# Performance work log

Hardware: AMD Instinct MI355X
Metric: run time of the kernel (lower is better)

## Reference

```python
import jax, jax.numpy as jnp
import numpy as np

# Constants matching init_kwargs
N_HEADS = 8
D_MODEL = 256
PATCH_NUM = 128
D_K = D_MODEL // N_HEADS  # 32
TEMP = 0.5
EPS = 1e-10


def setup_inputs() -> dict:
    key = jax.random.key(0)
    ks = jax.random.split(key, 20)
    s = 0.02
    d, h, n = D_MODEL, N_HEADS, PATCH_NUM
    inp = {
        "x": jax.random.normal(ks[0], (32, n, d), dtype=jnp.float32),
        "gumbel_u": jax.random.uniform(ks[1], (h, n, n, 2), dtype=jnp.float32),
        "memory_w": jax.random.normal(ks[2], (n, h * d), dtype=jnp.float32) * s,
        "fc_out_w": jax.random.normal(ks[3], (2 * d, d), dtype=jnp.float32) * s,
        "fc_out_b": jnp.zeros((d,), jnp.float32),
        "fc_cat_w": jax.random.normal(ks[4], (d, 2), dtype=jnp.float32) * s,
        "fc_cat_b": jnp.zeros((2,), jnp.float32),
        "wq": jax.random.normal(ks[5], (d, d), dtype=jnp.float32) * s,
        "bq": jnp.zeros((d,), jnp.float32),
        "wk": jax.random.normal(ks[6], (d, d), dtype=jnp.float32) * s,
        "bk": jnp.zeros((d,), jnp.float32),
        "wv": jax.random.normal(ks[7], (d, d), dtype=jnp.float32) * s,
        "bv": jnp.zeros((d,), jnp.float32),
        "out_w": jax.random.normal(ks[8], (d, d), dtype=jnp.float32) * s,
        "out_b": jnp.zeros((d,), jnp.float32),
        "mlp_w1": jax.random.normal(ks[9], (d, d), dtype=jnp.float32) * s,
        "mlp_b1": jnp.zeros((d,), jnp.float32),
        "mlp_w2": jax.random.normal(ks[10], (d, d), dtype=jnp.float32) * s,
        "mlp_b2": jnp.zeros((d,), jnp.float32),
    }
    return inp


def _forward(x, memory_w, fc_out_w, fc_out_b, fc_cat_w, fc_cat_b,
             wq, bq, wk, bk, wv, bv, out_w, out_b,
             mlp_w1, mlp_b1, mlp_w2, mlp_b2, gumbel_u):
    H, N, D = N_HEADS, PATCH_NUM, D_MODEL
    B = x.shape[0]

    # ---- SSConnectionLearning on memory feats ----
    # memory: Embedding(N, d_model*n_heads) -> feats [H, N, D]
    feats = memory_w.reshape(N, H, D).transpose(1, 0, 2)
    # rel_rec gathers row index i (receiver), rel_send gathers col index j (sender)
    senders = jnp.broadcast_to(feats[:, None, :, :], (H, N, N, D))   # feats[j]
    receivers = jnp.broadcast_to(feats[:, :, None, :], (H, N, N, D))  # feats[i]
    pair = jnp.concatenate([senders, receivers], axis=-1)  # [H,N,N,2D]
    hdn = jax.nn.relu(jnp.einsum('hijc,cd->hijd', pair, fc_out_w) + fc_out_b)
    logits = jnp.einsum('hijd,dk->hijk', hdn, fc_cat_w) + fc_cat_b  # [H,N,N,2]

    # gumbel-softmax, hard=True, straight-through
    g = -jnp.log(-jnp.log(gumbel_u + EPS) + EPS)
    y_soft = jax.nn.softmax((logits + g) / TEMP, axis=-1)
    y_hard = jax.nn.one_hot(jnp.argmax(y_soft, axis=-1), 2, dtype=y_soft.dtype)
    y = jax.lax.stop_gradient(y_hard - y_soft) + y_soft
    conn = y[..., 1]  # [H,N,N] learned sparse connection mask

    # ---- PatchIntegration (GELU MLP, dropout = identity in eval) ----
    xm = jax.nn.gelu(x @ mlp_w1 + mlp_b1)
    xm = xm @ mlp_w2 + mlp_b2

    # ---- Multihead attention masked by connection matrix ----
    q = (xm @ wq + bq).reshape(B, N, H, D_K).transpose(0, 2, 1, 3)  # [B,H,N,dk]
    k = (xm @ wk + bk).reshape(B, N, H, D_K).transpose(0, 2, 1, 3)
    v = (xm @ wv + bv).reshape(B, N, H, D_K).transpose(0, 2, 1, 3)
    scale = D_K ** -0.5
    scores = jnp.einsum('bhqd,bhkd->bhqk', q, k) * scale
    # additive mask: blocked where conn==0 (large negative keeps softmax finite)
    scores = scores + (conn[None] - 1.0) * 1e9
    attn = jax.nn.softmax(scores, axis=-1)
    out = jnp.einsum('bhqk,bhkd->bhqd', attn, v)
    out = out.transpose(0, 2, 1, 3).reshape(B, N, H * D_K)
    out = out @ out_w + out_b
    return out


def reference(x, gumbel_u, memory_w, fc_out_w, fc_out_b, fc_cat_w, fc_cat_b,
              wq, bq, wk, bk, wv, bv, out_w, out_b,
              mlp_w1, mlp_b1, mlp_w2, mlp_b2):
    return _forward(x, memory_w, fc_out_w, fc_out_b, fc_cat_w, fc_cat_b,
                    wq, bq, wk, bk, wv, bv, out_w, out_b,
                    mlp_w1, mlp_b1, mlp_w2, mlp_b2, gumbel_u)
```

## Files before the change

### kernel.cpp

```cpp
#include <hip/hip_runtime.h>
#include <hip/hip_bf16.h>
#include <math.h>


typedef short short8 __attribute__((ext_vector_type(8)));
typedef float f32x4 __attribute__((ext_vector_type(4)));

union V8 { uint4 u; short8 s; };

__device__ __forceinline__ float gelu_f(float x) {
    float inner = 0.7978845608028654f * (x + 0.044715f * x * x * x);
    return 0.5f * x * (1.0f + tanhf(inner));
}
__device__ __forceinline__ void split_bf16(float x, ushort& h, ushort& l) {
    __hip_bfloat16 bh = __float2bfloat16(x);
    float hf = __bfloat162float(bh);
    __hip_bfloat16 bl = __float2bfloat16(x - hf);
    h = __builtin_bit_cast(ushort, bh);
    l = __builtin_bit_cast(ushort, bl);
}
__device__ __forceinline__ ushort bf16bits(float x) {
    return __builtin_bit_cast(ushort, __float2bfloat16(x));
}
__device__ __forceinline__ float bits_to_f(ushort v) {
    return __builtin_bit_cast(float, ((uint)v) << 16);
}
__device__ __forceinline__ short8 lds_frag(const ushort* p) {
    V8 v; v.u = *(const uint4*)p; return v.s;
}


__global__ __launch_bounds__(512) void k_wprep(
    const float* __restrict__ mlp_w1, const float* __restrict__ mlp_w2,
    const float* __restrict__ wq, const float* __restrict__ wk,
    const float* __restrict__ wv, const float* __restrict__ out_w,
    const float* __restrict__ fc_out_w,
    ushort* __restrict__ hi, ushort* __restrict__ lo) {
    __shared__ __align__(16) float xs2[2][32 * 132];
    int bx = blockIdx.x, t = threadIdx.x;
    int half = t >> 8, tl = t & 255;
    int job = bx * 2 + half;
    int m = job >> 4, ks = (job >> 1) & 7, nh = job & 1;
    const float* W = m == 0 ? mlp_w1 : m == 1 ? mlp_w2 : m == 2 ? wq :
                     m == 3 ? wk : m == 4 ? wv : m == 5 ? out_w :
                     m == 6 ? fc_out_w : fc_out_w + 65536;
    ushort* Hm = hi + m * 65536;
    ushort* Lm = lo + m * 65536;
    float* xs = xs2[half];
    #pragma unroll
    for (int p = 0; p < 4; ++p) {
        int idx = p * 256 + tl;
        int row = idx >> 5, c4 = (idx & 31) * 4;
        *(float4*)(xs + row * 132 + c4) =
            *(const float4*)(W + (ks * 32 + row) * 256 + nh * 128 + c4);
    }
    __syncthreads();
    int lane = tl & 63, lr = lane & 15, quad = lane >> 4;
    #pragma unroll
    for (int it = 0; it < 2; ++it) {
        int tgl = (tl >> 6) + 4 * it;
        int tg = nh * 8 + tgl;
        int nl = tgl * 16 + lr;
        ushort hb[8], lb[8];
        #pragma unroll
        for (int j = 0; j < 8; ++j)
            split_bf16(xs[(quad * 8 + j) * 132 + nl], hb[j], lb[j]);
        uint4 ph = { (uint)hb[0] | ((uint)hb[1] << 16), (uint)hb[2] | ((uint)hb[3] << 16),
                     (uint)hb[4] | ((uint)hb[5] << 16), (uint)hb[6] | ((uint)hb[7] << 16) };
        uint4 pl = { (uint)lb[0] | ((uint)lb[1] << 16), (uint)lb[2] | ((uint)lb[3] << 16),
                     (uint)lb[4] | ((uint)lb[5] << 16), (uint)lb[6] | ((uint)lb[7] << 16) };
        int idx = ((tg * 8 + ks) * 64 + lane) * 8;
        *(uint4*)(Hm + idx) = ph;
        *(uint4*)(Lm + idx) = pl;
    }
}

__global__ __launch_bounds__(512) void k_p2(
    const float* __restrict__ memory_w, const float* __restrict__ X,
    const ushort* __restrict__ Whi, const ushort* __restrict__ Wlo,
    const float* __restrict__ b1, const float* __restrict__ b2,
    const float* __restrict__ Bq, const float* __restrict__ Bk,
    const float* __restrict__ Bv,
    float* __restrict__ A, float* __restrict__ Bm,
    ushort* __restrict__ Q, ushort* __restrict__ K, ushort* __restrict__ V) {
    __shared__ __align__(16) union {
        struct { ushort xhi[16 * 264], xlo[16 * 264]; } f;
        struct {
            ushort aHi[16 * 264], aLo[16 * 264];
            ushort bHi[16 * 264], bLo[16 * 264];
        } g;
    } sm;
    int bx = blockIdx.x, t = threadIdx.x;
    if (bx < 64) {
        int rt = bx;
        #pragma unroll
        for (int ii = 0; ii < 2; ++ii) {
            int f4 = ii * 512 + t;
            int rr = f4 >> 6, c = (f4 & 63) * 4;
            int r = rt * 16 + rr;
            int h = r >> 7, n = r & 127;
            float4 xv = *(const float4*)(memory_w + n * 2048 + h * 256 + c);
            ushort hh[4], ll[4];
            split_bf16(xv.x, hh[0], ll[0]); split_bf16(xv.y, hh[1], ll[1]);
            split_bf16(xv.z, hh[2], ll[2]); split_bf16(xv.w, hh[3], ll[3]);
            uint2 ph = { (uint)hh[0] | ((uint)hh[1] << 16), (uint)hh[2] | ((uint)hh[3] << 16) };
            uint2 pl = { (uint)ll[0] | ((uint)ll[1] << 16), (uint)ll[2] | ((uint)ll[3] << 16) };
            *(uint2*)(sm.f.xhi + rr * 264 + c) = ph;
            *(uint2*)(sm.f.xlo + rr * 264 + c) = pl;
        }
        __syncthreads();
        int lane = t & 63, w = t >> 6;
        int lr = lane & 15, quad = lane >> 4;
        int msel = w & 1, cq = w >> 1;
        const uint4* H4 = (const uint4*)(Whi + (6 + msel) * 65536);
        const uint4* L4 = (const uint4*)(Wlo + (6 + msel) * 65536);
        const ushort* ah = sm.f.xhi + lr * 264 + quad * 8;
        const ushort* al = sm.f.xlo + lr * 264 + quad * 8;
        float* O = msel ? Bm : A;
        #pragma unroll
        for (int i = 0; i < 4; ++i) {
            int tg = cq * 4 + i;
            f32x4 acc = {};
            #pragma unroll
            for (int ks = 0; ks < 8; ++ks) {
                short8 a_h = lds_frag(ah + ks * 32);
                short8 a_l = lds_frag(al + ks * 32);
                int off = (tg * 8 + ks) * 64 + lane;
                V8 bh, bl; bh.u = H4[off]; bl.u = L4[off];
                acc = __builtin_amdgcn_mfma_f32_16x16x32_bf16(a_h, bh.s, acc, 0, 0, 0);
                acc = __builtin_amdgcn_mfma_f32_16x16x32_bf16(a_l, bh.s, acc, 0, 0, 0);
                acc = __builtin_amdgcn_mfma_f32_16x16x32_bf16(a_h, bl.s, acc, 0, 0, 0);
            }
            int n0 = tg * 16 + lr;
            #pragma unroll
            for (int r = 0; r < 4; ++r)
                O[(rt * 16 + quad * 4 + r) * 256 + n0] = acc[r];
        }
        return;
    }
    int r0 = (bx - 64) * 16;
    #pragma unroll
    for (int ii = 0; ii < 2; ++ii) {
        int f4 = ii * 512 + t;
        int row = f4 >> 6, c = (f4 & 63) * 4;
        float4 xv = *(const float4*)(X + (r0 + row) * 256 + c);
        ushort h[4], l[4];
        split_bf16(xv.x, h[0], l[0]); split_bf16(xv.y, h[1], l[1]);
        split_bf16(xv.z, h[2], l[2]); split_bf16(xv.w, h[3], l[3]);
        uint2 ph = { (uint)h[0] | ((uint)h[1] << 16), (uint)h[2] | ((uint)h[3] << 16) };
        uint2 pl = { (uint)l[0] | ((uint)l[1] << 16), (uint)l[2] | ((uint)l[3] << 16) };
        *(uint2*)(sm.g.aHi + row * 264 + c) = ph;
        *(uint2*)(sm.g.aLo + row * 264 + c) = pl;
    }
    __syncthreads();
    int lane = t & 63, w = t >> 6;
    int lr = lane & 15, quad = lane >> 4;
    int aoff = lr * 264 + quad * 8;
    {
        const uint4* H4 = (const uint4*)(Whi + 0 * 65536);
        const uint4* L4 = (const uint4*)(Wlo + 0 * 65536);
        f32x4 acc[2] = {};
        #pragma unroll
        for (int ks = 0; ks < 8; ++ks) {
            short8 a_h = lds_frag(sm.g.aHi + aoff + ks * 32);
            short8 a_l = lds_frag(sm.g.aLo + aoff + ks * 32);
            #pragma unroll
            for (int ti = 0; ti < 2; ++ti) {
                int off = ((w * 2 + ti) * 8 + ks) * 64 + lane;
                V8 bh, bl; bh.u = H4[off]; bl.u = L4[off];
                acc[ti] = __builtin_amdgcn_mfma_f32_16x16x32_bf16(a_h, bh.s, acc[ti], 0, 0, 0);
                acc[ti] = __builtin_amdgcn_mfma_f32_16x16x32_bf16(a_l, bh.s, acc[ti], 0, 0, 0);
                acc[ti] = __builtin_amdgcn_mfma_f32_16x16x32_bf16(a_h, bl.s, acc[ti], 0, 0, 0);
            }
        }
        #pragma unroll
        for (int ti = 0; ti < 2; ++ti) {
            int n0 = (w * 2 + ti) * 16 + lr;
            float bb = b1[n0];
            #pragma unroll
            for (int r = 0; r < 4; ++r) {
                float o = gelu_f(acc[ti][r] + bb);
                ushort hh, ll; split_bf16(o, hh, ll);
                int ad = (quad * 4 + r) * 264 + n0;
                sm.g.bHi[ad] = hh; sm.g.bLo[ad] = ll;
            }
        }
    }
    __syncthreads();
    {
        const uint4* H4 = (const uint4*)(Whi + 1 * 65536);
        const uint4* L4 = (const uint4*)(Wlo + 1 * 65536);
        f32x4 acc[2] = {};
        #pragma unroll
        for (int ks = 0; ks < 8; ++ks) {
            short8 a_h = lds_frag(sm.g.bHi + aoff + ks * 32);
            short8 a_l = lds_frag(sm.g.bLo + aoff + ks * 32);
            #pragma unroll
            for (int ti = 0; ti < 2; ++ti) {
                int off = ((w * 2 + ti) * 8 + ks) * 64 + lane;
                V8 bh, bl; bh.u = H4[off]; bl.u = L4[off];
                acc[ti] = __builtin_amdgcn_mfma_f32_16x16x32_bf16(a_h, bh.s, acc[ti], 0, 0, 0);
                acc[ti] = __builtin_amdgcn_mfma_f32_16x16x32_bf16(a_l, bh.s, acc[ti], 0, 0, 0);
                acc[ti] = __builtin_amdgcn_mfma_f32_16x16x32_bf16(a_h, bl.s, acc[ti], 0, 0, 0);
            }
        }
        __syncthreads();
        #pragma unroll
        for (int ti = 0; ti < 2; ++ti) {
            int n0 = (w * 2 + ti) * 16 + lr;
            float bb = b2[n0];
            #pragma unroll
            for (int r = 0; r < 4; ++r) {
                float o = acc[ti][r] + bb;
                ushort hh, ll; split_bf16(o, hh, ll);
                int ad = (quad * 4 + r) * 264 + n0;
                sm.g.aHi[ad] = hh; sm.g.aLo[ad] = ll;
            }
        }
    }
    __syncthreads();
    {
        const uint4* Hq = (const uint4*)(Whi + 2 * 65536);
        const uint4* Lq = (const uint4*)(Wlo + 2 * 65536);
        const uint4* Hk = (const uint4*)(Whi + 3 * 65536);
        const uint4* Lk = (const uint4*)(Wlo + 3 * 65536);
        const uint4* Hv = (const uint4*)(Whi + 4 * 65536);
        const uint4* Lv = (const uint4*)(Wlo + 4 * 65536);
        f32x4 aq[2] = {}, ak[2] = {}, av[2] = {};
        #pragma unroll 2
        for (int ks = 0; ks < 8; ++ks) {
            short8 a_h = lds_frag(sm.g.aHi + aoff + ks * 32);
            short8 a_l = lds_frag(sm.g.aLo + aoff + ks * 32);
            #pragma unroll
            for (int ti = 0; ti < 2; ++ti) {
                int off = ((w * 2 + ti) * 8 + ks) * 64 + lane;
                V8 qh, ql, kh, kl, vh, vl;
                qh.u = Hq[off]; ql.u = Lq[off];
                kh.u = Hk[off]; kl.u = Lk[off];
                vh.u = Hv[off]; vl.u = Lv[off];
                aq[ti] = __builtin_amdgcn_mfma_f32_16x16x32_bf16(a_h, qh.s, aq[ti], 0, 0, 0);
                aq[ti] = __builtin_amdgcn_mfma_f32_16x16x32_bf16(a_l, qh.s, aq[ti], 0, 0, 0);
                aq[ti] = __builtin_amdgcn_mfma_f32_16x16x32_bf16(a_h, ql.s, aq[ti], 0, 0, 0);
                ak[ti] = __builtin_amdgcn_mfma_f32_16x16x32_bf16(a_h, kh.s, ak[ti], 0, 0, 0);
                ak[ti] = __builtin_amdgcn_mfma_f32_16x16x32_bf16(a_l, kh.s, ak[ti], 0, 0, 0);
                ak[ti] = __builtin_amdgcn_mfma_f32_16x16x32_bf16(a_h, kl.s, ak[ti], 0, 0, 0);
                av[ti] = __builtin_amdgcn_mfma_f32_16x16x32_bf16(a_h, vh.s, av[ti], 0, 0, 0);
                av[ti] = __builtin_amdgcn_mfma_f32_16x16x32_bf16(a_l, vh.s, av[ti], 0, 0, 0);
                av[ti] = __builtin_amdgcn_mfma_f32_16x16x32_bf16(a_h, vl.s, av[ti], 0, 0, 0);
            }
        }
        #pragma unroll
        for (int ti = 0; ti < 2; ++ti) {
            int n0 = (w * 2 + ti) * 16 + lr;
            float bq = Bq[n0], bk = Bk[n0], bv = Bv[n0];
            #pragma unroll
            for (int r = 0; r < 4; ++r) {
                int go = (r0 + quad * 4 + r) * 256 + n0;
                Q[go] = bf16bits(aq[ti][r] + bq);
                K[go] = bf16bits(ak[ti][r] + bk);
                V[go] = bf16bits(av[ti][r] + bv);
            }
        }
    }
}

__global__ __launch_bounds__(512) void k_conn(
    const float* __restrict__ A, const float* __restrict__ Bmat,
    const float* __restrict__ fc_out_b, const float* __restrict__ fc_cat_w,
    const float* __restrict__ fc_cat_b, const float* __restrict__ gumbel_u,
    ushort* __restrict__ maskb) {
    __shared__ __align__(16) float sA[16 * 260], sB[32 * 260];
    int bx = blockIdx.x, t = threadIdx.x;
    int h = bx >> 5;
    int rem = bx & 31;
    int it = rem >> 3, jt = rem & 7;
    int i0 = it * 32, j0 = jt * 16;
    int jl = t & 15, il = t >> 4;
    #pragma unroll
    for (int p = 0; p < 6; ++p) {
        int id2 = p * 512 + t;
        if (id2 < 1024) {
            int rr = id2 >> 6, c = (id2 & 63) * 4;
            *(float4*)(sA + rr * 260 + c) =
                *(const float4*)(A + (h * 128 + j0 + rr) * 256 + c);
        } else {
            int id3 = id2 - 1024;
            int rr = id3 >> 6, c = (id3 & 63) * 4;
            float4 bv = *(const float4*)(Bmat + (h * 128 + i0 + rr) * 256 + c);
            float4 fb = *(const float4*)(fc_out_b + c);
            bv.x += fb.x; bv.y += fb.y; bv.z += fb.z; bv.w += fb.w;
            *(float4*)(sB + rr * 260 + c) = bv;
        }
    }
    __syncthreads();
    const float* Ar = sA + jl * 260;
    const float* Br = sB + il * 260;
    float l0 = fc_cat_b[0], l1 = fc_cat_b[1];
    #pragma unroll 4
    for (int d4 = 0; d4 < 64; ++d4) {
        int d = d4 * 4;
        float4 av = *(const float4*)(Ar + d);
        float4 bv = *(const float4*)(Br + d);
        float4 cwA = *(const float4*)(fc_cat_w + d * 2);
        float4 cwB = *(const float4*)(fc_cat_w + d * 2 + 4);
        float h0 = fmaxf(av.x + bv.x, 0.f);
        float h1 = fmaxf(av.y + bv.y, 0.f);
        float h2 = fmaxf(av.z + bv.z, 0.f);
        float h3 = fmaxf(av.w + bv.w, 0.f);
        l0 += h0 * cwA.x + h1 * cwA.z + h2 * cwB.x + h3 * cwB.z;
        l1 += h0 * cwA.y + h1 * cwA.w + h2 * cwB.y + h3 * cwB.w;
    }
    int i = i0 + il, j = j0 + jl;
    float2 uu = *(const float2*)(gumbel_u + ((h * 128 + i) * 128 + j) * 2);
    float g0 = -logf(-logf(uu.x + 1e-10f) + 1e-10f);
    float g1 = -logf(-logf(uu.y + 1e-10f) + 1e-10f);
    bool on = (l1 + g1) > (l0 + g0);
    maskb[(h * 128 + i) * 128 + j] = bf16bits(on ? 0.f : -1e9f);
}

__global__ __launch_bounds__(256) void k_attn_mfma(
    const ushort* __restrict__ Q, const ushort* __restrict__ K,
    const ushort* __restrict__ V, const ushort* __restrict__ maskb,
    float* __restrict__ AO) {
    int bx = blockIdx.x;
    int b = bx >> 4, h = (bx >> 1) & 7, rh = bx & 1;
    int t = threadIdx.x;
    int lane = t & 63, w = t >> 6;
    __shared__ __align__(16) ushort vT[32 * 136];
    __shared__ __align__(16) ushort ps[64 * 136];
    #pragma unroll
    for (int it = 0; it < 2; ++it) {
        int idx = it * 256 + t;
        int key = idx >> 2, dq8 = (idx & 3) * 8;
        V8 vv; vv.u = *(const uint4*)(V + (b * 128 + key) * 256 + h * 32 + dq8);
        #pragma unroll
        for (int m = 0; m < 8; ++m)
            vT[(dq8 + m) * 136 + key] = (ushort)vv.s[m];
    }
    __syncthreads();
    int lr = lane & 15, quad = lane >> 4;
    int rt = rh * 4 + w;
    V8 af;
    af.u = *(const uint4*)(Q + (b * 128 + rt * 16 + lr) * 256 + h * 32 + quad * 8);
    f32x4 s[8];
    #pragma unroll
    for (int ct = 0; ct < 8; ++ct) {
        V8 bf_;
        bf_.u = *(const uint4*)(K + (b * 128 + ct * 16 + lr) * 256 + h * 32 + quad * 8);
        f32x4 z = {0.f, 0.f, 0.f, 0.f};
        s[ct] = __builtin_amdgcn_mfma_f32_16x16x32_bf16(af.s, bf_.s, z, 0, 0, 0);
    }
    const float scale = 0.17677669529663687f;
    const ushort* mrow = maskb + h * 16384;
    #pragma unroll
    for (int r = 0; r < 4; ++r) {
        int lrow = w * 16 + quad * 4 + r;
        int grow = rt * 16 + quad * 4 + r;
        float sv[8];
        float mx = -3.0e38f;
        #pragma unroll
        for (int ct = 0; ct < 8; ++ct) {
            float bias = bits_to_f(mrow[grow * 128 + ct * 16 + lr]);
            sv[ct] = s[ct][r] * scale + bias;
            mx = fmaxf(mx, sv[ct]);
        }
        mx = fmaxf(mx, __shfl_xor(mx, 1));
        mx = fmaxf(mx, __shfl_xor(mx, 2));
        mx = fmaxf(mx, __shfl_xor(mx, 4));
        mx = fmaxf(mx, __shfl_xor(mx, 8));
        float sum = 0.f;
        #pragma unroll
        for (int ct = 0; ct < 8; ++ct) {
            sv[ct] = __expf(sv[ct] - mx);
            sum += sv[ct];
        }
        sum += __shfl_xor(sum, 1);
        sum += __shfl_xor(sum, 2);
        sum += __shfl_xor(sum, 4);
        sum += __shfl_xor(sum, 8);
        float iv = 1.f / sum;
        #pragma unroll
        for (int ct = 0; ct < 8; ++ct)
            ps[lrow * 136 + ct * 16 + lr] = bf16bits(sv[ct] * iv);
    }
    f32x4 o0 = {}, o1 = {};
    #pragma unroll
    for (int kk = 0; kk < 4; ++kk) {
        short8 pa = lds_frag(ps + (w * 16 + lr) * 136 + kk * 32 + quad * 8);
        short8 v0 = lds_frag(vT + lr * 136 + kk * 32 + quad * 8);
        short8 v1 = lds_frag(vT + (16 + lr) * 136 + kk * 32 + quad * 8);
        o0 = __builtin_amdgcn_mfma_f32_16x16x32_bf16(pa, v0, o0, 0, 0, 0);
        o1 = __builtin_amdgcn_mfma_f32_16x16x32_bf16(pa, v1, o1, 0, 0, 0);
    }
    #pragma unroll
    for (int r = 0; r < 4; ++r) {
        int grow = rt * 16 + quad * 4 + r;
        float* op = AO + b * 32768 + grow * 256 + h * 32;
        op[lr] = o0[r];
        op[16 + lr] = o1[r];
    }
}

__global__ __launch_bounds__(256) void k_gemm16(
    const float* __restrict__ X, const ushort* __restrict__ Whi,
    const ushort* __restrict__ Wlo, const float* __restrict__ bias,
    float* __restrict__ Y) {
    __shared__ __align__(16) ushort xhi[16 * 264], xlo[16 * 264];
    int t = threadIdx.x;
    int r0 = blockIdx.x * 16;
    #pragma unroll
    for (int ii = 0; ii < 4; ++ii) {
        int f4 = ii * 256 + t;
        int row = f4 >> 6, c = (f4 & 63) * 4;
        float4 xv = *(const float4*)(X + (r0 + row) * 256 + c);
        ushort h[4], l[4];
        split_bf16(xv.x, h[0], l[0]); split_bf16(xv.y, h[1], l[1]);
        split_bf16(xv.z, h[2], l[2]); split_bf16(xv.w, h[3], l[3]);
        uint2 ph = { (uint)h[0] | ((uint)h[1] << 16), (uint)h[2] | ((uint)h[3] << 16) };
        uint2 pl = { (uint)l[0] | ((uint)l[1] << 16), (uint)l[2] | ((uint)l[3] << 16) };
        *(uint2*)(xhi + row * 264 + c) = ph;
        *(uint2*)(xlo + row * 264 + c) = pl;
    }
    __syncthreads();
    int l = t & 63, w = t >> 6;
    int lr = l & 15, quad = l >> 4;
    int tg = blockIdx.y * 4 + w;
    const ushort* ah = xhi + lr * 264 + quad * 8;
    const ushort* al = xlo + lr * 264 + quad * 8;
    const uint4* H4 = (const uint4*)Whi;
    const uint4* L4 = (const uint4*)Wlo;
    f32x4 acc = {};
    #pragma unroll
    for (int ks = 0; ks < 8; ++ks) {
        short8 a_h = lds_frag(ah + ks * 32);
        short8 a_l = lds_frag(al + ks * 32);
        int off = (tg * 8 + ks) * 64 + l;
        V8 bh, bl; bh.u = H4[off]; bl.u = L4[off];
        acc = __builtin_amdgcn_mfma_f32_16x16x32_bf16(a_h, bh.s, acc, 0, 0, 0);
        acc = __builtin_amdgcn_mfma_f32_16x16x32_bf16(a_l, bh.s, acc, 0, 0, 0);
        acc = __builtin_amdgcn_mfma_f32_16x16x32_bf16(a_h, bl.s, acc, 0, 0, 0);
    }
    int n0 = tg * 16 + lr;
    float bs = bias[n0];
    #pragma unroll
    for (int r = 0; r < 4; ++r)
        Y[(r0 + quad * 4 + r) * 256 + n0] = acc[r] + bs;
}

extern "C" void kernel_launch(void* const* d_in, const int* in_sizes, int n_in,
                              void* d_out, int out_size, void* d_ws, size_t ws_size,
                              hipStream_t stream) {
    const float* x        = (const float*)d_in[0];
    const float* gumbel_u = (const float*)d_in[1];
    const float* memory_w = (const float*)d_in[2];
    const float* fc_out_w = (const float*)d_in[3];
    const float* fc_out_b = (const float*)d_in[4];
    const float* fc_cat_w = (const float*)d_in[5];
    const float* fc_cat_b = (const float*)d_in[6];
    const float* wq       = (const float*)d_in[7];
    const float* bq       = (const float*)d_in[8];
    const float* wk       = (const float*)d_in[9];
    const float* bk       = (const float*)d_in[10];
    const float* wv_      = (const float*)d_in[11];
    const float* bv_      = (const float*)d_in[12];
    const float* out_w    = (const float*)d_in[13];
    const float* out_b    = (const float*)d_in[14];
    const float* mlp_w1   = (const float*)d_in[15];
    const float* mlp_b1   = (const float*)d_in[16];
    const float* mlp_w2   = (const float*)d_in[17];
    const float* mlp_b2   = (const float*)d_in[18];

    float* ws    = (float*)d_ws;
    float* A     = ws;
    float* Bm    = ws + 262144;
    ushort* mask = (ushort*)(ws + 524288);
    ushort* qb   = (ushort*)(ws + 589824);
    ushort* kb   = (ushort*)(ws + 1114112);
    ushort* vb   = (ushort*)(ws + 1638400);
    float* ao    = ws + 2162688;
    ushort* wf_hi = (ushort*)(ws + 3211264);
    ushort* wf_lo = wf_hi + 8 * 65536;
    float* out   = (float*)d_out;

    k_wprep<<<dim3(64), dim3(512), 0, stream>>>(
        mlp_w1, mlp_w2, wq, wk, wv_, out_w, fc_out_w, wf_hi, wf_lo);
    k_p2<<<dim3(320), dim3(512), 0, stream>>>(
        memory_w, x, wf_hi, wf_lo, mlp_b1, mlp_b2, bq, bk, bv_,
        A, Bm, qb, kb, vb);
    k_conn<<<dim3(256), dim3(512), 0, stream>>>(
        A, Bm, fc_out_b, fc_cat_w, fc_cat_b, gumbel_u, mask);
    k_attn_mfma<<<dim3(512), dim3(256), 0, stream>>>(qb, kb, vb, mask, ao);
    k_gemm16<<<dim3(256, 4), dim3(256), 0, stream>>>(ao, wf_hi + 5 * 65536,
                                                     wf_lo + 5 * 65536, out_b, out);
}
```

Before: 144.7 us.

## Regroup kernels: merge weight prep with memory GEMM, fuse MLP/QKV with conn mask

The launch sequence is restructured from five kernels into four. The first kernel now splits the six square weights into bf16 hi/lo and also computes the memory-feature GEMMs (A, Bm), reading and splitting fc_out_w directly from fp32 in-loop instead of using pre-split weights. The second kernel runs the MLP/QKV projection and the connection-mask computation as independent block ranges, which removes one launch and one dependency barrier. The cost is strided, uncoalesced fp32 loads of fc_out_w with redundant splitting in the memory GEMM blocks, and a larger union in shared memory for the fused kernel.

```diff
diff --git a/kernel.cpp b/kernel.cpp
--- a/kernel.cpp
+++ b/kernel.cpp
@@ -30,69 +30,55 @@
 }
 
 
-__global__ __launch_bounds__(512) void k_wprep(
+__global__ __launch_bounds__(512) void k_d1(
     const float* __restrict__ mlp_w1, const float* __restrict__ mlp_w2,
     const float* __restrict__ wq, const float* __restrict__ wk,
     const float* __restrict__ wv, const float* __restrict__ out_w,
-    const float* __restrict__ fc_out_w,
-    ushort* __restrict__ hi, ushort* __restrict__ lo) {
-    __shared__ __align__(16) float xs2[2][32 * 132];
-    int bx = blockIdx.x, t = threadIdx.x;
-    int half = t >> 8, tl = t & 255;
-    int job = bx * 2 + half;
-    int m = job >> 4, ks = (job >> 1) & 7, nh = job & 1;
-    const float* W = m == 0 ? mlp_w1 : m == 1 ? mlp_w2 : m == 2 ? wq :
-                     m == 3 ? wk : m == 4 ? wv : m == 5 ? out_w :
-                     m == 6 ? fc_out_w : fc_out_w + 65536;
-    ushort* Hm = hi + m * 65536;
-    ushort* Lm = lo + m * 65536;
-    float* xs = xs2[half];
-    #pragma unroll
-    for (int p = 0; p < 4; ++p) {
-        int idx = p * 256 + tl;
-        int row = idx >> 5, c4 = (idx & 31) * 4;
-        *(float4*)(xs + row * 132 + c4) =
-            *(const float4*)(W + (ks * 32 + row) * 256 + nh * 128 + c4);
-    }
-    __syncthreads();
-    int lane = tl & 63, lr = lane & 15, quad = lane >> 4;
-    #pragma unroll
-    for (int it = 0; it < 2; ++it) {
-        int tgl = (tl >> 6) + 4 * it;
-        int tg = nh * 8 + tgl;
-        int nl = tgl * 16 + lr;
-        ushort hb[8], lb[8];
-        #pragma unroll
-        for (int j = 0; j < 8; ++j)
-            split_bf16(xs[(quad * 8 + j) * 132 + nl], hb[j], lb[j]);
-        uint4 ph = { (uint)hb[0] | ((uint)hb[1] << 16), (uint)hb[2] | ((uint)hb[3] << 16),
-                     (uint)hb[4] | ((uint)hb[5] << 16), (uint)hb[6] | ((uint)hb[7] << 16) };
-        uint4 pl = { (uint)lb[0] | ((uint)lb[1] << 16), (uint)lb[2] | ((uint)lb[3] << 16),
-                     (uint)lb[4] | ((uint)lb[5] << 16), (uint)lb[6] | ((uint)lb[7] << 16) };
-        int idx = ((tg * 8 + ks) * 64 + lane) * 8;
-        *(uint4*)(Hm + idx) = ph;
-        *(uint4*)(Lm + idx) = pl;
-    }
-}
-
-__global__ __launch_bounds__(512) void k_p2(
-    const float* __restrict__ memory_w, const float* __restrict__ X,
-    const ushort* __restrict__ Whi, const ushort* __restrict__ Wlo,
-    const float* __restrict__ b1, const float* __restrict__ b2,
-    const float* __restrict__ Bq, const float* __restrict__ Bk,
-    const float* __restrict__ Bv,
-    float* __restrict__ A, float* __restrict__ Bm,
-    ushort* __restrict__ Q, ushort* __restrict__ K, ushort* __restrict__ V) {
+    const float* __restrict__ fc_out_w, const float* __restrict__ memory_w,
+    ushort* __restrict__ hi, ushort* __restrict__ lo,
+    float* __restrict__ A, float* __restrict__ Bm) {
     __shared__ __align__(16) union {
+        float xs[2][32 * 132];
         struct { ushort xhi[16 * 264], xlo[16 * 264]; } f;
-        struct {
-            ushort aHi[16 * 264], aLo[16 * 264];
-            ushort bHi[16 * 264], bLo[16 * 264];
-        } g;
     } sm;
     int bx = blockIdx.x, t = threadIdx.x;
-    if (bx < 64) {
-        int rt = bx;
+    if (bx < 48) {
+        int half = t >> 8, tl = t & 255;
+        int job = bx * 2 + half;
+        int m = job >> 4, ks = (job >> 1) & 7, nh = job & 1;
+        const float* W = m == 0 ? mlp_w1 : m == 1 ? mlp_w2 : m == 2 ? wq :
+                         m == 3 ? wk : m == 4 ? wv : out_w;
+        ushort* Hm = hi + m * 65536;
+        ushort* Lm = lo + m * 65536;
+        float* xs = sm.xs[half];
+        #pragma unroll
+        for (int p = 0; p < 4; ++p) {
+            int idx = p * 256 + tl;
+            int row = idx >> 5, c4 = (idx & 31) * 4;
+            *(float4*)(xs + row * 132 + c4) =
+                *(const float4*)(W + (ks * 32 + row) * 256 + nh * 128 + c4);
+        }
+        __syncthreads();
+        int lane = tl & 63, lr = lane & 15, quad = lane >> 4;
+        #pragma unroll
+        for (int it = 0; it < 2; ++it) {
+            int tgl = (tl >> 6) + 4 * it;
+            int tg = nh * 8 + tgl;
+            int nl = tgl * 16 + lr;
+            ushort hb[8], lb[8];
+            #pragma unroll
+            for (int j = 0; j < 8; ++j)
+                split_bf16(xs[(quad * 8 + j) * 132 + nl], hb[j], lb[j]);
+            uint4 ph = { (uint)hb[0] | ((uint)hb[1] << 16), (uint)hb[2] | ((uint)hb[3] << 16),
+                         (uint)hb[4] | ((uint)hb[5] << 16), (uint)hb[6] | ((uint)hb[7] << 16) };
+            uint4 pl = { (uint)lb[0] | ((uint)lb[1] << 16), (uint)lb[2] | ((uint)lb[3] << 16),
+                         (uint)lb[4] | ((uint)lb[5] << 16), (uint)lb[6] | ((uint)lb[7] << 16) };
+            int idx = ((tg * 8 + ks) * 64 + lane) * 8;
+            *(uint4*)(Hm + idx) = ph;
+            *(uint4*)(Lm + idx) = pl;
+        }
+    } else {
+        int rt = bx - 48;
         #pragma unroll
         for (int ii = 0; ii < 2; ++ii) {
             int f4 = ii * 512 + t;
@@ -112,210 +98,231 @@
         int lane = t & 63, w = t >> 6;
         int lr = lane & 15, quad = lane >> 4;
         int msel = w & 1, cq = w >> 1;
-        const uint4* H4 = (const uint4*)(Whi + (6 + msel) * 65536);
-        const uint4* L4 = (const uint4*)(Wlo + (6 + msel) * 65536);
+        const float* Wf = fc_out_w + msel * 65536;
         const ushort* ah = sm.f.xhi + lr * 264 + quad * 8;
         const ushort* al = sm.f.xlo + lr * 264 + quad * 8;
         float* O = msel ? Bm : A;
         #pragma unroll
         for (int i = 0; i < 4; ++i) {
             int tg = cq * 4 + i;
+            int n = tg * 16 + lr;
             f32x4 acc = {};
             #pragma unroll
             for (int ks = 0; ks < 8; ++ks) {
                 short8 a_h = lds_frag(ah + ks * 32);
                 short8 a_l = lds_frag(al + ks * 32);
-                int off = (tg * 8 + ks) * 64 + lane;
-                V8 bh, bl; bh.u = H4[off]; bl.u = L4[off];
+                int k0 = ks * 32 + quad * 8;
+                V8 bh, bl;
+                #pragma unroll
+                for (int j = 0; j < 8; ++j) {
+                    ushort hh, ll;
+                    split_bf16(Wf[(k0 + j) * 256 + n], hh, ll);
+                    bh.s[j] = (short)hh;
+                    bl.s[j] = (short)ll;
+                }
                 acc = __builtin_amdgcn_mfma_f32_16x16x32_bf16(a_h, bh.s, acc, 0, 0, 0);
                 acc = __builtin_amdgcn_mfma_f32_16x16x32_bf16(a_l, bh.s, acc, 0, 0, 0);
                 acc = __builtin_amdgcn_mfma_f32_16x16x32_bf16(a_h, bl.s, acc, 0, 0, 0);
             }
-            int n0 = tg * 16 + lr;
             #pragma unroll
             for (int r = 0; r < 4; ++r)
-                O[(rt * 16 + quad * 4 + r) * 256 + n0] = acc[r];
-        }
-        return;
-    }
-    int r0 = (bx - 64) * 16;
-    #pragma unroll
-    for (int ii = 0; ii < 2; ++ii) {
-        int f4 = ii * 512 + t;
-        int row = f4 >> 6, c = (f4 & 63) * 4;
-        float4 xv = *(const float4*)(X + (r0 + row) * 256 + c);
-        ushort h[4], l[4];
-        split_bf16(xv.x, h[0], l[0]); split_bf16(xv.y, h[1], l[1]);
-        split_bf16(xv.z, h[2], l[2]); split_bf16(xv.w, h[3], l[3]);
-        uint2 ph = { (uint)h[0] | ((uint)h[1] << 16), (uint)h[2] | ((uint)h[3] << 16) };
-        uint2 pl = { (uint)l[0] | ((uint)l[1] << 16), (uint)l[2] | ((uint)l[3] << 16) };
-        *(uint2*)(sm.g.aHi + row * 264 + c) = ph;
-        *(uint2*)(sm.g.aLo + row * 264 + c) = pl;
-    }
-    __syncthreads();
-    int lane = t & 63, w = t >> 6;
-    int lr = lane & 15, quad = lane >> 4;
-    int aoff = lr * 264 + quad * 8;
-    {
-        const uint4* H4 = (const uint4*)(Whi + 0 * 65536);
-        const uint4* L4 = (const uint4*)(Wlo + 0 * 65536);
-        f32x4 acc[2] = {};
-        #pragma unroll
-        for (int ks = 0; ks < 8; ++ks) {
-            short8 a_h = lds_frag(sm.g.aHi + aoff + ks * 32);
-            short8 a_l = lds_frag(sm.g.aLo + aoff + ks * 32);
-            #pragma unroll
-            for (int ti = 0; ti < 2; ++ti) {
-                int off = ((w * 2 + ti) * 8 + ks) * 64 + lane;
-                V8 bh, bl; bh.u = H4[off]; bl.u = L4[off];
-                acc[ti] = __builtin_amdgcn_mfma_f32_16x16x32_bf16(a_h, bh.s, acc[ti], 0, 0, 0);
-                acc[ti] = __builtin_amdgcn_mfma_f32_16x16x32_bf16(a_l, bh.s, acc[ti], 0, 0, 0);
-                acc[ti] = __builtin_amdgcn_mfma_f32_16x16x32_bf16(a_h, bl.s, acc[ti], 0, 0, 0);
-            }
-        }
-        #pragma unroll
-        for (int ti = 0; ti < 2; ++ti) {
-            int n0 = (w * 2 + ti) * 16 + lr;
-            float bb = b1[n0];
-            #pragma unroll
-            for (int r = 0; r < 4; ++r) {
-                float o = gelu_f(acc[ti][r] + bb);
-                ushort hh, ll; split_bf16(o, hh, ll);
-                int ad = (quad * 4 + r) * 264 + n0;
-                sm.g.bHi[ad] = hh; sm.g.bLo[ad] = ll;
-            }
-        }
-    }
-    __syncthreads();
-    {
-        const uint4* H4 = (const uint4*)(Whi + 1 * 65536);
-        const uint4* L4 = (const uint4*)(Wlo + 1 * 65536);
-        f32x4 acc[2] = {};
-        #pragma unroll
-        for (int ks = 0; ks < 8; ++ks) {
-            short8 a_h = lds_frag(sm.g.bHi + aoff + ks * 32);
-            short8 a_l = lds_frag(sm.g.bLo + aoff + ks * 32);
-            #pragma unroll
-            for (int ti = 0; ti < 2; ++ti) {
-                int off = ((w * 2 + ti) * 8 + ks) * 64 + lane;
-                V8 bh, bl; bh.u = H4[off]; bl.u = L4[off];
-                acc[ti] = __builtin_amdgcn_mfma_f32_16x16x32_bf16(a_h, bh.s, acc[ti], 0, 0, 0);
-                acc[ti] = __builtin_amdgcn_mfma_f32_16x16x32_bf16(a_l, bh.s, acc[ti], 0, 0, 0);
-                acc[ti] = __builtin_amdgcn_mfma_f32_16x16x32_bf16(a_h, bl.s, acc[ti], 0, 0, 0);
-            }
-        }
-        __syncthreads();
-        #pragma unroll
-        for (int ti = 0; ti < 2; ++ti) {
-            int n0 = (w * 2 + ti) * 16 + lr;
-            float bb = b2[n0];
-            #pragma unroll
-            for (int r = 0; r < 4; ++r) {
-                float o = acc[ti][r] + bb;
-                ushort hh, ll; split_bf16(o, hh, ll);
-                int ad = (quad * 4 + r) * 264 + n0;
-                sm.g.aHi[ad] = hh; sm.g.aLo[ad] = ll;
-            }
-        }
-    }
-    __syncthreads();
-    {
-        const uint4* Hq = (const uint4*)(Whi + 2 * 65536);
-        const uint4* Lq = (const uint4*)(Wlo + 2 * 65536);
-        const uint4* Hk = (const uint4*)(Whi + 3 * 65536);
-        const uint4* Lk = (const uint4*)(Wlo + 3 * 65536);
-        const uint4* Hv = (const uint4*)(Whi + 4 * 65536);
-        const uint4* Lv = (const uint4*)(Wlo + 4 * 65536);
-        f32x4 aq[2] = {}, ak[2] = {}, av[2] = {};
-        #pragma unroll 2
-        for (int ks = 0; ks < 8; ++ks) {
-            short8 a_h = lds_frag(sm.g.aHi + aoff + ks * 32);
-            short8 a_l = lds_frag(sm.g.aLo + aoff + ks * 32);
-            #pragma unroll
-            for (int ti = 0; ti < 2; ++ti) {
-                int off = ((w * 2 + ti) * 8 + ks) * 64 + lane;
-                V8 qh, ql, kh, kl, vh, vl;
-                qh.u = Hq[off]; ql.u = Lq[off];
-                kh.u = Hk[off]; kl.u = Lk[off];
-                vh.u = Hv[off]; vl.u = Lv[off];
-                aq[ti] = __builtin_amdgcn_mfma_f32_16x16x32_bf16(a_h, qh.s, aq[ti], 0, 0, 0);
-                aq[ti] = __builtin_amdgcn_mfma_f32_16x16x32_bf16(a_l, qh.s, aq[ti], 0, 0, 0);
-                aq[ti] = __builtin_amdgcn_mfma_f32_16x16x32_bf16(a_h, ql.s, aq[ti], 0, 0, 0);
-                ak[ti] = __builtin_amdgcn_mfma_f32_16x16x32_bf16(a_h, kh.s, ak[ti], 0, 0, 0);
-                ak[ti] = __builtin_amdgcn_mfma_f32_16x16x32_bf16(a_l, kh.s, ak[ti], 0, 0, 0);
-                ak[ti] = __builtin_amdgcn_mfma_f32_16x16x32_bf16(a_h, kl.s, ak[ti], 0, 0, 0);
-                av[ti] = __builtin_amdgcn_mfma_f32_16x16x32_bf16(a_h, vh.s, av[ti], 0, 0, 0);
-                av[ti] = __builtin_amdgcn_mfma_f32_16x16x32_bf16(a_l, vh.s, av[ti], 0, 0, 0);
-                av[ti] = __builtin_amdgcn_mfma_f32_16x16x32_bf16(a_h, vl.s, av[ti], 0, 0, 0);
-            }
-        }
-        #pragma unroll
-        for (int ti = 0; ti < 2; ++ti) {
-            int n0 = (w * 2 + ti) * 16 + lr;
-            float bq = Bq[n0], bk = Bk[n0], bv = Bv[n0];
-            #pragma unroll
-            for (int r = 0; r < 4; ++r) {
-                int go = (r0 + quad * 4 + r) * 256 + n0;
-                Q[go] = bf16bits(aq[ti][r] + bq);
-                K[go] = bf16bits(ak[ti][r] + bk);
-                V[go] = bf16bits(av[ti][r] + bv);
-            }
-        }
-    }
-}
-
-__global__ __launch_bounds__(512) void k_conn(
+                O[(rt * 16 + quad * 4 + r) * 256 + n] = acc[r];
+        }
+    }
+}
+
+__global__ __launch_bounds__(512) void k_d2(
+    const float* __restrict__ X,
+    const ushort* __restrict__ Whi, const ushort* __restrict__ Wlo,
+    const float* __restrict__ b1, const float* __restrict__ b2,
+    const float* __restrict__ Bq, const float* __restrict__ Bk,
+    const float* __restrict__ Bv,
+    ushort* __restrict__ Q, ushort* __restrict__ K, ushort* __restrict__ V,
     const float* __restrict__ A, const float* __restrict__ Bmat,
     const float* __restrict__ fc_out_b, const float* __restrict__ fc_cat_w,
     const float* __restrict__ fc_cat_b, const float* __restrict__ gumbel_u,
     ushort* __restrict__ maskb) {
-    __shared__ __align__(16) float sA[16 * 260], sB[32 * 260];
+    __shared__ __align__(16) union {
+        struct {
+            ushort aHi[16 * 264], aLo[16 * 264];
+            ushort bHi[16 * 264], bLo[16 * 264];
+        } g;
+        struct { float sA[16 * 260]; float sB[32 * 260]; } c;
+    } sm;
     int bx = blockIdx.x, t = threadIdx.x;
-    int h = bx >> 5;
-    int rem = bx & 31;
-    int it = rem >> 3, jt = rem & 7;
-    int i0 = it * 32, j0 = jt * 16;
-    int jl = t & 15, il = t >> 4;
-    #pragma unroll
-    for (int p = 0; p < 6; ++p) {
-        int id2 = p * 512 + t;
-        if (id2 < 1024) {
-            int rr = id2 >> 6, c = (id2 & 63) * 4;
-            *(float4*)(sA + rr * 260 + c) =
-                *(const float4*)(A + (h * 128 + j0 + rr) * 256 + c);
-        } else {
-            int id3 = id2 - 1024;
-            int rr = id3 >> 6, c = (id3 & 63) * 4;
-            float4 bv = *(const float4*)(Bmat + (h * 128 + i0 + rr) * 256 + c);
-            float4 fb = *(const float4*)(fc_out_b + c);
-            bv.x += fb.x; bv.y += fb.y; bv.z += fb.z; bv.w += fb.w;
-            *(float4*)(sB + rr * 260 + c) = bv;
-        }
-    }
-    __syncthreads();
-    const float* Ar = sA + jl * 260;
-    const float* Br = sB + il * 260;
-    float l0 = fc_cat_b[0], l1 = fc_cat_b[1];
-    #pragma unroll 4
-    for (int d4 = 0; d4 < 64; ++d4) {
-        int d = d4 * 4;
-        float4 av = *(const float4*)(Ar + d);
-        float4 bv = *(const float4*)(Br + d);
-        float4 cwA = *(const float4*)(fc_cat_w + d * 2);
-        float4 cwB = *(const float4*)(fc_cat_w + d * 2 + 4);
-        float h0 = fmaxf(av.x + bv.x, 0.f);
-        float h1 = fmaxf(av.y + bv.y, 0.f);
-        float h2 = fmaxf(av.z + bv.z, 0.f);
-        float h3 = fmaxf(av.w + bv.w, 0.f);
-        l0 += h0 * cwA.x + h1 * cwA.z + h2 * cwB.x + h3 * cwB.z;
-        l1 += h0 * cwA.y + h1 * cwA.w + h2 * cwB.y + h3 * cwB.w;
-    }
-    int i = i0 + il, j = j0 + jl;
-    float2 uu = *(const float2*)(gumbel_u + ((h * 128 + i) * 128 + j) * 2);
-    float g0 = -logf(-logf(uu.x + 1e-10f) + 1e-10f);
-    float g1 = -logf(-logf(uu.y + 1e-10f) + 1e-10f);
-    bool on = (l1 + g1) > (l0 + g0);
-    maskb[(h * 128 + i) * 128 + j] = bf16bits(on ? 0.f : -1e9f);
+    if (bx < 256) {
+        int r0 = bx * 16;
+        #pragma unroll
+        for (int ii = 0; ii < 2; ++ii) {
+            int f4 = ii * 512 + t;
+            int row = f4 >> 6, c = (f4 & 63) * 4;
+            float4 xv = *(const float4*)(X + (r0 + row) * 256 + c);
+            ushort h[4], l[4];
+            split_bf16(xv.x, h[0], l[0]); split_bf16(xv.y, h[1], l[1]);
+            split_bf16(xv.z, h[2], l[2]); split_bf16(xv.w, h[3], l[3]);
+            uint2 ph = { (uint)h[0] | ((uint)h[1] << 16), (uint)h[2] | ((uint)h[3] << 16) };
+            uint2 pl = { (uint)l[0] | ((uint)l[1] << 16), (uint)l[2] | ((uint)l[3] << 16) };
+            *(uint2*)(sm.g.aHi + row * 264 + c) = ph;
+            *(uint2*)(sm.g.aLo + row * 264 + c) = pl;
+        }
+        __syncthreads();
+        int lane = t & 63, w = t >> 6;
+        int lr = lane & 15, quad = lane >> 4;
+        int aoff = lr * 264 + quad * 8;
+        {
+            const uint4* H4 = (const uint4*)(Whi + 0 * 65536);
+            const uint4* L4 = (const uint4*)(Wlo + 0 * 65536);
+            f32x4 acc[2] = {};
+            #pragma unroll
+            for (int ks = 0; ks < 8; ++ks) {
+                short8 a_h = lds_frag(sm.g.aHi + aoff + ks * 32);
+                short8 a_l = lds_frag(sm.g.aLo + aoff + ks * 32);
+                #pragma unroll
+                for (int ti = 0; ti < 2; ++ti) {
+                    int off = ((w * 2 + ti) * 8 + ks) * 64 + lane;
+                    V8 bh, bl; bh.u = H4[off]; bl.u = L4[off];
+                    acc[ti] = __builtin_amdgcn_mfma_f32_16x16x32_bf16(a_h, bh.s, acc[ti], 0, 0, 0);
+                    acc[ti] = __builtin_amdgcn_mfma_f32_16x16x32_bf16(a_l, bh.s, acc[ti], 0, 0, 0);
+                    acc[ti] = __builtin_amdgcn_mfma_f32_16x16x32_bf16(a_h, bl.s, acc[ti], 0, 0, 0);
+                }
+            }
+            #pragma unroll
+            for (int ti = 0; ti < 2; ++ti) {
+                int n0 = (w * 2 + ti) * 16 + lr;
+                float bb = b1[n0];
+                #pragma unroll
+                for (int r = 0; r < 4; ++r) {
+                    float o = gelu_f(acc[ti][r] + bb);
+                    ushort hh, ll; split_bf16(o, hh, ll);
+                    int ad = (quad * 4 + r) * 264 + n0;
+                    sm.g.bHi[ad] = hh; sm.g.bLo[ad] = ll;
+                }
+            }
+        }
+        __syncthreads();
+        {
+            const uint4* H4 = (const uint4*)(Whi + 1 * 65536);
+            const uint4* L4 = (const uint4*)(Wlo + 1 * 65536);
+            f32x4 acc[2] = {};
+            #pragma unroll
+            for (int ks = 0; ks < 8; ++ks) {
+                short8 a_h = lds_frag(sm.g.bHi + aoff + ks * 32);
+                short8 a_l = lds_frag(sm.g.bLo + aoff + ks * 32);
+                #pragma unroll
+                for (int ti = 0; ti < 2; ++ti) {
+                    int off = ((w * 2 + ti) * 8 + ks) * 64 + lane;
+                    V8 bh, bl; bh.u = H4[off]; bl.u = L4[off];
+                    acc[ti] = __builtin_amdgcn_mfma_f32_16x16x32_bf16(a_h, bh.s, acc[ti], 0, 0, 0);
+                    acc[ti] = __builtin_amdgcn_mfma_f32_16x16x32_bf16(a_l, bh.s, acc[ti], 0, 0, 0);
+                    acc[ti] = __builtin_amdgcn_mfma_f32_16x16x32_bf16(a_h, bl.s, acc[ti], 0, 0, 0);
+                }
+            }
+            __syncthreads();
+            #pragma unroll
+            for (int ti = 0; ti < 2; ++ti) {
+                int n0 = (w * 2 + ti) * 16 + lr;
+                float bb = b2[n0];
+                #pragma unroll
+                for (int r = 0; r < 4; ++r) {
+                    float o = acc[ti][r] + bb;
+                    ushort hh, ll; split_bf16(o, hh, ll);
+                    int ad = (quad * 4 + r) * 264 + n0;
+                    sm.g.aHi[ad] = hh; sm.g.aLo[ad] = ll;
+                }
+            }
+        }
+        __syncthreads();
+        {
+            const uint4* Hq = (const uint4*)(Whi + 2 * 65536);
+            const uint4* Lq = (const uint4*)(Wlo + 2 * 65536);
+            const uint4* Hk = (const uint4*)(Whi + 3 * 65536);
+            const uint4* Lk = (const uint4*)(Wlo + 3 * 65536);
+            const uint4* Hv = (const uint4*)(Whi + 4 * 65536);
+            const uint4* Lv = (const uint4*)(Wlo + 4 * 65536);
+            f32x4 aq[2] = {}, ak[2] = {}, av[2] = {};
+            #pragma unroll 2
+            for (int ks = 0; ks < 8; ++ks) {
+                short8 a_h = lds_frag(sm.g.aHi + aoff + ks * 32);
+                short8 a_l = lds_frag(sm.g.aLo + aoff + ks * 32);
+                #pragma unroll
+                for (int ti = 0; ti < 2; ++ti) {
+                    int off = ((w * 2 + ti) * 8 + ks) * 64 + lane;
+                    V8 qh, ql, kh, kl, vh, vl;
+                    qh.u = Hq[off]; ql.u = Lq[off];
+                    kh.u = Hk[off]; kl.u = Lk[off];
+                    vh.u = Hv[off]; vl.u = Lv[off];
+                    aq[ti] = __builtin_amdgcn_mfma_f32_16x16x32_bf16(a_h, qh.s, aq[ti], 0, 0, 0);
+                    aq[ti] = __builtin_amdgcn_mfma_f32_16x16x32_bf16(a_l, qh.s, aq[ti], 0, 0, 0);
+                    aq[ti] = __builtin_amdgcn_mfma_f32_16x16x32_bf16(a_h, ql.s, aq[ti], 0, 0, 0);
+                    ak[ti] = __builtin_amdgcn_mfma_f32_16x16x32_bf16(a_h, kh.s, ak[ti], 0, 0, 0);
+                    ak[ti] = __builtin_amdgcn_mfma_f32_16x16x32_bf16(a_l, kh.s, ak[ti], 0, 0, 0);
+                    ak[ti] = __builtin_amdgcn_mfma_f32_16x16x32_bf16(a_h, kl.s, ak[ti], 0, 0, 0);
+                    av[ti] = __builtin_amdgcn_mfma_f32_16x16x32_bf16(a_h, vh.s, av[ti], 0, 0, 0);
+                    av[ti] = __builtin_amdgcn_mfma_f32_16x16x32_bf16(a_l, vh.s, av[ti], 0, 0, 0);
+                    av[ti] = __builtin_amdgcn_mfma_f32_16x16x32_bf16(a_h, vl.s, av[ti], 0, 0, 0);
+                }
+            }
+            #pragma unroll
+            for (int ti = 0; ti < 2; ++ti) {
+                int n0 = (w * 2 + ti) * 16 + lr;
+                float bq = Bq[n0], bk = Bk[n0], bv = Bv[n0];
+                #pragma unroll
+                for (int r = 0; r < 4; ++r) {
+                    int go = (r0 + quad * 4 + r) * 256 + n0;
+                    Q[go] = bf16bits(aq[ti][r] + bq);
+                    K[go] = bf16bits(ak[ti][r] + bk);
+                    V[go] = bf16bits(av[ti][r] + bv);
+                }
+            }
+        }
+    } else {
+        int idx = bx - 256;
+        int h = idx >> 5;
+        int rem = idx & 31;
+        int it = rem >> 3, jt = rem & 7;
+        int i0 = it * 32, j0 = jt * 16;
+        int jl = t & 15, il = t >> 4;
+        #pragma unroll
+        for (int p = 0; p < 6; ++p) {
+            int id2 = p * 512 + t;
+            if (id2 < 1024) {
+                int rr = id2 >> 6, c = (id2 & 63) * 4;
+                *(float4*)(sm.c.sA + rr * 260 + c) =
+                    *(const float4*)(A + (h * 128 + j0 + rr) * 256 + c);
+            } else {
+                int id3 = id2 - 1024;
+                int rr = id3 >> 6, c = (id3 & 63) * 4;
+                float4 bv = *(const float4*)(Bmat + (h * 128 + i0 + rr) * 256 + c);
+                float4 fb = *(const float4*)(fc_out_b + c);
+                bv.x += fb.x; bv.y += fb.y; bv.z += fb.z; bv.w += fb.w;
+                *(float4*)(sm.c.sB + rr * 260 + c) = bv;
+            }
+        }
+        __syncthreads();
+        const float* Ar = sm.c.sA + jl * 260;
+        const float* Br = sm.c.sB + il * 260;
+        float l0 = fc_cat_b[0], l1 = fc_cat_b[1];
+        #pragma unroll 4
+        for (int d4 = 0; d4 < 64; ++d4) {
+            int d = d4 * 4;
+            float4 av = *(const float4*)(Ar + d);
+            float4 bv = *(const float4*)(Br + d);
+            float4 cwA = *(const float4*)(fc_cat_w + d * 2);
+            float4 cwB = *(const float4*)(fc_cat_w + d * 2 + 4);
+            float h0 = fmaxf(av.x + bv.x, 0.f);
+            float h1 = fmaxf(av.y + bv.y, 0.f);
+            float h2 = fmaxf(av.z + bv.z, 0.f);
+            float h3 = fmaxf(av.w + bv.w, 0.f);
+            l0 += h0 * cwA.x + h1 * cwA.z + h2 * cwB.x + h3 * cwB.z;
+            l1 += h0 * cwA.y + h1 * cwA.w + h2 * cwB.y + h3 * cwB.w;
+        }
+        int i = i0 + il, j = j0 + jl;
+        float2 uu = *(const float2*)(gumbel_u + ((h * 128 + i) * 128 + j) * 2);
+        float g0 = -logf(-logf(uu.x + 1e-10f) + 1e-10f);
+        float g1 = -logf(-logf(uu.y + 1e-10f) + 1e-10f);
+        bool on = (l1 + g1) > (l0 + g0);
+        maskb[(h * 128 + i) * 128 + j] = bf16bits(on ? 0.f : -1e9f);
+    }
 }
 
 __global__ __launch_bounds__(256) void k_attn_mfma(
@@ -482,12 +489,11 @@
     ushort* wf_lo = wf_hi + 8 * 65536;
     float* out   = (float*)d_out;
 
-    k_wprep<<<dim3(64), dim3(512), 0, stream>>>(
-        mlp_w1, mlp_w2, wq, wk, wv_, out_w, fc_out_w, wf_hi, wf_lo);
-    k_p2<<<dim3(320), dim3(512), 0, stream>>>(
-        memory_w, x, wf_hi, wf_lo, mlp_b1, mlp_b2, bq, bk, bv_,
-        A, Bm, qb, kb, vb);
-    k_conn<<<dim3(256), dim3(512), 0, stream>>>(
+    k_d1<<<dim3(112), dim3(512), 0, stream>>>(
+        mlp_w1, mlp_w2, wq, wk, wv_, out_w, fc_out_w, memory_w,
+        wf_hi, wf_lo, A, Bm);
+    k_d2<<<dim3(512), dim3(512), 0, stream>>>(
+        x, wf_hi, wf_lo, mlp_b1, mlp_b2, bq, bk, bv_, qb, kb, vb,
         A, Bm, fc_out_b, fc_cat_w, fc_cat_b, gumbel_u, mask);
     k_attn_mfma<<<dim3(512), dim3(256), 0, stream>>>(qb, kb, vb, mask, ao);
     k_gemm16<<<dim3(256, 4), dim3(256), 0, stream>>>(ao, wf_hi + 5 * 65536,
```

After: 151.3 us. +4.6%, slower.
